# Optimization experiments

Hardware: AMD Instinct MI355X
Metric: run time of the kernel (lower is better)

Reference implementation:

```python
import jax, jax.numpy as jnp
import numpy as np

N_NODES = 100000
N_EDGES = 1600000
DIM = 64


def setup_inputs() -> dict:
    key = jax.random.key(0)
    ks = jax.random.split(key, 10)
    return {
        "h_real": jax.random.normal(ks[0], (N_NODES, DIM), dtype=jnp.float32),
        "h_imag": jax.random.normal(ks[1], (N_NODES, DIM), dtype=jnp.float32),
        "d": jax.random.uniform(ks[2], (N_NODES,), dtype=jnp.float32),
        "w_real": jax.random.normal(ks[3], (N_EDGES,), dtype=jnp.float32),
        "w_imag": jax.random.normal(ks[4], (N_EDGES,), dtype=jnp.float32),
        "src": jax.random.randint(ks[5], (N_EDGES,), 0, N_NODES, dtype=jnp.int32),
        "dst": jax.random.randint(ks[6], (N_EDGES,), 0, N_NODES, dtype=jnp.int32),
        "W1": jax.random.normal(ks[7], (DIM, DIM), dtype=jnp.float32) * (1.414 / np.sqrt(DIM)),
        "b1": jnp.zeros((DIM,), dtype=jnp.float32),
        "W2": jax.random.normal(ks[8], (DIM, DIM), dtype=jnp.float32) * (1.414 / np.sqrt(DIM)),
        "b2": jnp.zeros((DIM,), dtype=jnp.float32),
    }


def reference(h_real, h_imag, d, w_real, w_imag, src, dst, W1, b1, W2, b2):
    n = h_real.shape[0]
    # per-edge complex coefficient e = d_dst * d_src * (w_real + i w_imag)
    dd = d[dst] * d[src]                      # [E]
    e_r = (dd * w_real)[:, None]              # [E,1]
    e_i = (dd * w_imag)[:, None]              # [E,1]
    hr = h_real[src]                          # [E,D]
    hi = h_imag[src]                          # [E,D]
    # complex multiply e * h, fused single pass over edges
    m_r = e_r * hr - e_i * hi                 # [E,D]
    m_i = e_i * hr + e_r * hi                 # [E,D]
    z_real = jax.ops.segment_sum(m_r, dst, num_segments=n)  # [N,D]
    z_imag = jax.ops.segment_sum(m_i, dst, num_segments=n)  # [N,D]
    # note: original overwrites z_real first, then z_imag uses the NEW z_real
    zr = (z_real @ W1.T + b1) - (z_imag @ W2.T + b2)
    zi = (zr @ W2.T + b2) + (z_imag @ W1.T + b1)
    return zr, zi
```

## Files before the change

### kernel.cpp

```cpp
#include <hip/hip_runtime.h>
#include <hip/hip_bf16.h>

#define N_NODES 100000
#define N_EDGES 1600000
#define DIM 64

#define TILE 4096
#define B1 ((N_EDGES + TILE - 1) / TILE)
#define K1 ((N_NODES + 255) / 256)
#define NCOUNTS (K1 * B1)
#define SCAN_BLOCK 1024
#define NSB ((NCOUNTS + SCAN_BLOCK - 1) / SCAN_BLOCK)
#define PACKB4 ((N_NODES * DIM / 4 + 255) / 256)
#define PLACE_CAP 4736
#define NPW 8
#define PULLB (N_NODES / 32)

typedef __attribute__((ext_vector_type(8))) short bf16x8;
typedef __attribute__((ext_vector_type(4))) float f32x4;

#if defined(__has_builtin)
#if __has_builtin(__builtin_amdgcn_fdot2_f32_bf16)
#define HAVE_DOT2 1
typedef __attribute__((ext_vector_type(2))) __bf16 bf16x2v;
#endif
#endif


__device__ __forceinline__ unsigned pack_bf16x2(float lo, float hi) {
  unsigned ulo = (unsigned)__hip_bfloat16_raw(__float2bfloat16(lo)).x;
  unsigned uhi = (unsigned)__hip_bfloat16_raw(__float2bfloat16(hi)).x;
  return ulo | (uhi << 16);
}
__device__ __forceinline__ float unpack_lo(unsigned u) {
  return __int_as_float((int)(u << 16));
}
__device__ __forceinline__ float unpack_hi(unsigned u) {
  return __int_as_float((int)(u & 0xFFFF0000u));
}
__device__ __forceinline__ unsigned short f2bf(float x) {
  return __hip_bfloat16_raw(__float2bfloat16(x)).x;
}

__global__ __launch_bounds__(256) void setup_fused_kernel(
    const float* __restrict__ h_real, const float* __restrict__ h_imag,
    unsigned* __restrict__ hpack, const float* __restrict__ W1,
    const float* __restrict__ b1, const float* __restrict__ W2,
    const float* __restrict__ b2, unsigned short* __restrict__ At,
    float* __restrict__ cvec, const int* __restrict__ dst,
    int* __restrict__ counts) {
  const int bid = blockIdx.x;
  const int tid = threadIdx.x;
  if (bid < PACKB4) {
    const int i = bid * 256 + tid;
    const float4 hr = ((const float4*)h_real)[i];
    const float4 hi = ((const float4*)h_imag)[i];
    uint4 o;
    o.x = pack_bf16x2(hr.x, hi.x);
    o.y = pack_bf16x2(hr.y, hi.y);
    o.z = pack_bf16x2(hr.z, hi.z);
    o.w = pack_bf16x2(hr.w, hi.w);
    ((uint4*)hpack)[i] = o;
    return;
  }
  if (bid < PACKB4 + 64) {
    const int idx = (bid - PACKB4) * 256 + tid;
    if (idx < 128 * 128) {
      const int n = idx >> 7, k = idx & 127;
      float v;
      if (n < 64) {
        v = (k < 64) ? W1[n * 64 + k] : -W2[n * 64 + (k - 64)];
      } else {
        const int nn = n - 64;
        if (k < 64) {
          float s = 0.0f;
          for (int j = 0; j < 64; ++j) s += W1[j * 64 + k] * W2[nn * 64 + j];
          v = s;
        } else {
          const int kk = k - 64;
          float s = 0.0f;
          for (int j = 0; j < 64; ++j) s += W2[j * 64 + kk] * W2[nn * 64 + j];
          v = W1[nn * 64 + kk] - s;
        }
      }
      At[n * 128 + k] = f2bf(v);
    }
    if (idx < 128) {
      if (idx < 64) {
        cvec[idx] = b1[idx] - b2[idx];
      } else {
        const int nn = idx - 64;
        float s = 0.0f;
        for (int j = 0; j < 64; ++j) s += (b1[j] - b2[j]) * W2[nn * 64 + j];
        cvec[idx] = s + b1[nn] + b2[nn];
      }
    }
    return;
  }
  __shared__ int lh[K1];
  const int hb = bid - PACKB4 - 64;
  for (int i = tid; i < K1; i += 256) lh[i] = 0;
  __syncthreads();
  const int e0 = hb * TILE;
  const int e1 = min(e0 + TILE, N_EDGES);
  for (int e = e0 + tid; e < e1; e += 256) atomicAdd(&lh[dst[e] >> 8], 1);
  __syncthreads();
  for (int b = tid; b < K1; b += 256) counts[b * B1 + hb] = lh[b];
}

__global__ __launch_bounds__(SCAN_BLOCK) void scan1_kernel(
    int* __restrict__ cnt, int* __restrict__ bsum) {
  __shared__ int wsum[16];
  const int tid = threadIdx.x;
  const int lane = tid & 63;
  const int w = tid >> 6;
  const int i = blockIdx.x * SCAN_BLOCK + tid;
  const int orig = (i < NCOUNTS) ? cnt[i] : 0;
  int v = orig;
#pragma unroll
  for (int off = 1; off < 64; off <<= 1) {
    int t = __shfl_up(v, off);
    if (lane >= off) v += t;
  }
  if (lane == 63) wsum[w] = v;
  __syncthreads();
  if (w == 0) {
    int s = (lane < 16) ? wsum[lane] : 0;
#pragma unroll
    for (int off = 1; off < 16; off <<= 1) {
      int t = __shfl_up(s, off);
      if (lane >= off) s += t;
    }
    if (lane < 16) wsum[lane] = s;
  }
  __syncthreads();
  const int wex = (w == 0) ? 0 : wsum[w - 1];
  if (i < NCOUNTS) cnt[i] = wex + v - orig;
  if (tid == SCAN_BLOCK - 1) bsum[blockIdx.x] = wex + v;
}

__global__ __launch_bounds__(256) void scan2_kernel(
    const int* __restrict__ bsum, int* __restrict__ bpre) {
  __shared__ int wsum[4];
  const int tid = threadIdx.x;
  const int lane = tid & 63;
  const int w = tid >> 6;
  const int orig = (tid < NSB) ? bsum[tid] : 0;
  int v = orig;
#pragma unroll
  for (int off = 1; off < 64; off <<= 1) {
    int t = __shfl_up(v, off);
    if (lane >= off) v += t;
  }
  if (lane == 63) wsum[w] = v;
  __syncthreads();
  if (w == 0) {
    int s = (lane < 4) ? wsum[lane] : 0;
#pragma unroll
    for (int off = 1; off < 4; off <<= 1) {
      int t = __shfl_up(s, off);
      if (lane >= off) s += t;
    }
    if (lane < 4) wsum[lane] = s;
  }
  __syncthreads();
  const int wex = (w == 0) ? 0 : wsum[w - 1];
  if (tid < NSB) bpre[tid] = wex + v - orig;
}

__global__ __launch_bounds__(512) void partition_kernel(
    const int* __restrict__ src, const int* __restrict__ dst,
    const float* __restrict__ dvec,
    const float* __restrict__ w_real, const float* __restrict__ w_imag,
    const int* __restrict__ coffs, const int* __restrict__ bpre,
    unsigned long long* __restrict__ records) {
  __shared__ unsigned long long stage[TILE];
  __shared__ unsigned short sb[TILE];
  __shared__ int lhist[512];
  __shared__ int lbase[K1];
  __shared__ int lcur[K1];
  __shared__ int gbase[K1];
  __shared__ int wsum[8];
  const int tid = threadIdx.x;
  const int lane = tid & 63;
  const int w = tid >> 6;
  const int blk = blockIdx.x;
  const int e0 = blk * TILE;
  const int cnt_t = min(TILE, N_EDGES - e0);

  lhist[tid] = 0;
  __syncthreads();
  for (int j = tid; j < cnt_t; j += 512) atomicAdd(&lhist[dst[e0 + j] >> 8], 1);
  __syncthreads();
  const int myc = lhist[tid];
  int v = myc;
#pragma unroll
  for (int off = 1; off < 64; off <<= 1) {
    int t = __shfl_up(v, off);
    if (lane >= off) v += t;
  }
  if (lane == 63) wsum[w] = v;
  __syncthreads();
  if (w == 0) {
    int s = (lane < 8) ? wsum[lane] : 0;
#pragma unroll
    for (int off = 1; off < 8; off <<= 1) {
      int t = __shfl_up(s, off);
      if (lane >= off) s += t;
    }
    if (lane < 8) wsum[lane] = s;
  }
  __syncthreads();
  const int ex = v + ((w == 0) ? 0 : wsum[w - 1]) - myc;
  if (tid < K1) {
    lbase[tid] = ex;
    lcur[tid] = ex;
    const int ci = tid * B1 + blk;
    gbase[tid] = coffs[ci] + bpre[ci >> 10];
  }
  __syncthreads();

  for (int j = tid; j < cnt_t; j += 512) {
    const int e = e0 + j;
    const int t = dst[e];
    const int s = src[e];
    const int b = t >> 8;
    const float ds = dvec[s];
    const unsigned lo = (unsigned)s | ((unsigned)(t & 255) << 17);
    const unsigned hi = pack_bf16x2(ds * w_real[e], ds * w_imag[e]);
    const int r = atomicAdd(&lcur[b], 1);
    stage[r] = ((unsigned long long)hi << 32) | lo;
    sb[r] = (unsigned short)b;
  }
  __syncthreads();
  for (int i = tid; i < cnt_t; i += 512) {
    const int b = sb[i];
    records[gbase[b] + (i - lbase[b])] = stage[i];
  }
}

__global__ __launch_bounds__(256) void place_kernel(
    unsigned long long* __restrict__ records, const int* __restrict__ coffs,
    const int* __restrict__ bpre, int* __restrict__ inc) {
  const int b = blockIdx.x;
  const int tid = threadIdx.x;
  const int lane = tid & 63;
  const int w = tid >> 6;
  const int ci0 = b * B1;
  const int bstart = coffs[ci0] + bpre[ci0 >> 10];
  int bend;
  if (b == K1 - 1) {
    bend = N_EDGES;
  } else {
    const int ci1 = (b + 1) * B1;
    bend = coffs[ci1] + bpre[ci1 >> 10];
  }
  const int cnt = min(bend - bstart, PLACE_CAP);
  const int nbase = b << 8;
  const int nn = min(256, N_NODES - nbase);

  __shared__ unsigned long long stage[PLACE_CAP];
  __shared__ int ncnt[256];
  __shared__ int ncur[256];
  __shared__ int wsum[4];

  ncnt[tid] = 0;
  __syncthreads();
  for (int i = tid; i < cnt; i += 256) {
    const unsigned long long rec = records[bstart + i];
    stage[i] = rec;
    atomicAdd(&ncnt[((unsigned)rec >> 17) & 255], 1);
  }
  __syncthreads();
  const int myc = ncnt[tid];
  int v = myc;
#pragma unroll
  for (int off = 1; off < 64; off <<= 1) {
    int t = __shfl_up(v, off);
    if (lane >= off) v += t;
  }
  if (lane == 63) wsum[w] = v;
  __syncthreads();
  if (w == 0) {
    int s = (lane < 4) ? wsum[lane] : 0;
#pragma unroll
    for (int off = 1; off < 4; off <<= 1) {
      int t = __shfl_up(s, off);
      if (lane >= off) s += t;
    }
    if (lane < 4) wsum[lane] = s;
  }
  __syncthreads();
  const int incl = v + ((w == 0) ? 0 : wsum[w - 1]);
  const int base = bstart + incl - myc;
  ncur[tid] = base;
  if (tid < nn) inc[nbase + tid] = base + myc;
  __syncthreads();
  for (int i = tid; i < cnt; i += 256) {
    const unsigned long long rec = stage[i];
    const int pos = atomicAdd(&ncur[((unsigned)rec >> 17) & 255], 1);
    records[pos] = rec;
  }
}

__global__ __launch_bounds__(256, 8) void pull_fused_kernel(
    const uint2* __restrict__ records, const int* __restrict__ inc,
    const float* __restrict__ dvec, const unsigned* __restrict__ hpack,
    const unsigned short* __restrict__ At, const float* __restrict__ cvec,
    float* __restrict__ zr_out, float* __restrict__ zi_out) {
  __shared__ __align__(16) unsigned short zs[32][136];
  const int tid = threadIdx.x;
  const int lane = tid & 63;
  const int wave = tid >> 6;
  const int q4 = lane >> 4;
  const int m16 = lane & 15;
  const int node0 = blockIdx.x * 32;
  const unsigned* __restrict__ hb = hpack + 4 * m16;

#if HAVE_DOT2
#define DOT2(acc, w_, h_)                                                   \
  acc = __builtin_amdgcn_fdot2_f32_bf16(__builtin_bit_cast(bf16x2v, (w_)),  \
                                        __builtin_bit_cast(bf16x2v, (h_)),  \
                                        acc, false)
#else
#define DOT2(acc, w_, h_)                                                   \
  {                                                                         \
    const float _wl = unpack_lo(w_), _wh = unpack_hi(w_);                   \
    const float _hl = unpack_lo(h_), _hh = unpack_hi(h_);                   \
    acc += _wl * _hl + _wh * _hh;                                           \
  }
#endif

#define ACC4(RR)                                                            \
  {                                                                         \
    const unsigned wneg = (RR).y ^ 0x80000000u;                             \
    const unsigned wswp = ((RR).y >> 16) | ((RR).y << 16);                  \
    const uint4 hv = *reinterpret_cast<const uint4*>(                       \
        hb + (size_t)((RR).x & 0x1FFFF) * DIM);                             \
    DOT2(sr0, wneg, hv.x); DOT2(si0, wswp, hv.x);                           \
    DOT2(sr1, wneg, hv.y); DOT2(si1, wswp, hv.y);                           \
    DOT2(sr2, wneg, hv.z); DOT2(si2, wswp, hv.z);                           \
    DOT2(sr3, wneg, hv.w); DOT2(si3, wswp, hv.w);                           \
  }

  for (int j = 0; j < NPW; ++j) {
    const int n = node0 + wave * NPW + j;
    const int start = (n == 0) ? 0 : inc[n - 1];
    const int end = inc[n];
    const int deg = end - start;

    float sr0 = 0.f, sr1 = 0.f, sr2 = 0.f, sr3 = 0.f;
    float si0 = 0.f, si1 = 0.f, si2 = 0.f, si3 = 0.f;

    int p = start + q4;
    const int nfull = deg >> 2;
    int i = 0;
    for (; i + 2 <= nfull; i += 2) {
      const uint2 r0 = records[p];
      const uint2 r1 = records[p + 4];
      ACC4(r0);
      ACC4(r1);
      p += 8;
    }
    if (i < nfull) {
      const uint2 r0 = records[p];
      ACC4(r0);
      p += 4;
    }
    if (p < end) {
      const uint2 r0 = records[p];
      ACC4(r0);
    }

#define QRED(v)                  \
    v += __shfl_xor(v, 16);      \
    v += __shfl_xor(v, 32);
    QRED(sr0) QRED(sr1) QRED(sr2) QRED(sr3)
    QRED(si0) QRED(si1) QRED(si2) QRED(si3)
#undef QRED

    const float dn = dvec[n];
    if (lane < 16) {
      const int zl = wave * NPW + j;
      uint2 rv, iv;
      rv.x = pack_bf16x2(dn * sr0, dn * sr1);
      rv.y = pack_bf16x2(dn * sr2, dn * sr3);
      iv.x = pack_bf16x2(dn * si0, dn * si1);
      iv.y = pack_bf16x2(dn * si2, dn * si3);
      *reinterpret_cast<uint2*>(&zs[zl][4 * lane]) = rv;
      *reinterpret_cast<uint2*>(&zs[zl][64 + 4 * lane]) = iv;
    }
  }
#undef ACC4
#undef DOT2
  __syncthreads();

  {
    const int m = lane & 15;
    const int q = lane >> 4;
#pragma unroll
    for (int kk = 0; kk < 4; ++kk) {
      const int tt = wave + kk * 4;
      const int nh = tt >> 3;
      const int ft = tt & 7;

      bf16x8 a[4];
#pragma unroll
      for (int c = 0; c < 4; ++c)
        a[c] = *reinterpret_cast<const bf16x8*>(&zs[nh * 16 + m][c * 32 + q * 8]);

      f32x4 acc = (f32x4){0.f, 0.f, 0.f, 0.f};
      const unsigned short* brow = At + (size_t)(ft * 16 + m) * 128 + q * 8;
#pragma unroll
      for (int c = 0; c < 4; ++c) {
        bf16x8 bfrag = *reinterpret_cast<const bf16x8*>(brow + c * 32);
        acc = __builtin_amdgcn_mfma_f32_16x16x32_bf16(a[c], bfrag, acc, 0, 0, 0);
      }

      const int nf = ft * 16 + m;
      const float bias = cvec[nf];
      float* outp = (nf < 64) ? zr_out : zi_out;
      const int nnn = nf & 63;
#pragma unroll
      for (int r = 0; r < 4; ++r) {
        const int node = node0 + nh * 16 + q * 4 + r;
        outp[(size_t)node * 64 + nnn] = acc[r] + bias;
      }
    }
  }
}

extern "C" void kernel_launch(void* const* d_in, const int* in_sizes, int n_in,
                              void* d_out, int out_size, void* d_ws, size_t ws_size,
                              hipStream_t stream) {
  const float* h_real = (const float*)d_in[0];
  const float* h_imag = (const float*)d_in[1];
  const float* dvec   = (const float*)d_in[2];
  const float* w_real = (const float*)d_in[3];
  const float* w_imag = (const float*)d_in[4];
  const int*   src    = (const int*)d_in[5];
  const int*   dst    = (const int*)d_in[6];
  const float* W1     = (const float*)d_in[7];
  const float* b1     = (const float*)d_in[8];
  const float* W2     = (const float*)d_in[9];
  const float* b2     = (const float*)d_in[10];

  char* ws = (char*)d_ws;
  unsigned short* At = (unsigned short*)ws;
  float* cvec = (float*)(ws + 128 * 128 * 2);
  unsigned long long* records = (unsigned long long*)(ws + 33792);
  unsigned* hpack = (unsigned*)(ws + 33792 + (size_t)N_EDGES * 8);
  int* counts = (int*)(ws + 33792 + (size_t)N_EDGES * 8 + (size_t)N_NODES * DIM * 4);
  int* bsum = counts + NCOUNTS;
  int* bpre = bsum + NSB;
  int* inc  = bpre + NSB;

  float* zr_out = (float*)d_out;
  float* zi_out = zr_out + (size_t)N_NODES * DIM;

  setup_fused_kernel<<<PACKB4 + 64 + B1, 256, 0, stream>>>(
      h_real, h_imag, (unsigned*)hpack, W1, b1, W2, b2, At, cvec, dst, counts);
  scan1_kernel<<<NSB, SCAN_BLOCK, 0, stream>>>(counts, bsum);
  scan2_kernel<<<1, 256, 0, stream>>>(bsum, bpre);
  partition_kernel<<<B1, 512, 0, stream>>>(src, dst, dvec, w_real, w_imag,
                                           counts, bpre, records);
  place_kernel<<<K1, 256, 0, stream>>>(records, counts, bpre, inc);
  pull_fused_kernel<<<PULLB, 256, 0, stream>>>(
      (const uint2*)records, inc, dvec, hpack, At, cvec, zr_out, zi_out);
}
```

Measured before the change: 271.7 us.

## Restructure pull kernel: 16 nodes per 512-thread block, deeper gather unroll, staged stores

Result: faster. 265.1 us (-2.4%).

```diff
diff --git a/kernel.cpp b/kernel.cpp
--- a/kernel.cpp
+++ b/kernel.cpp
@@ -13,8 +13,7 @@
 #define NSB ((NCOUNTS + SCAN_BLOCK - 1) / SCAN_BLOCK)
 #define PACKB4 ((N_NODES * DIM / 4 + 255) / 256)
 #define PLACE_CAP 4736
-#define NPW 8
-#define PULLB (N_NODES / 32)
+#define PULLB (N_NODES / 16)
 
 typedef __attribute__((ext_vector_type(8))) short bf16x8;
 typedef __attribute__((ext_vector_type(4))) float f32x4;
@@ -303,18 +302,19 @@
   }
 }
 
-__global__ __launch_bounds__(256, 8) void pull_fused_kernel(
+__global__ __launch_bounds__(512, 8) void pull_fused_kernel(
     const uint2* __restrict__ records, const int* __restrict__ inc,
     const float* __restrict__ dvec, const unsigned* __restrict__ hpack,
     const unsigned short* __restrict__ At, const float* __restrict__ cvec,
     float* __restrict__ zr_out, float* __restrict__ zi_out) {
-  __shared__ __align__(16) unsigned short zs[32][136];
+  __shared__ __align__(16) unsigned short zs[16][136];
+  __shared__ __align__(16) float outbuf[16][132];
   const int tid = threadIdx.x;
   const int lane = tid & 63;
   const int wave = tid >> 6;
   const int q4 = lane >> 4;
   const int m16 = lane & 15;
-  const int node0 = blockIdx.x * 32;
+  const int node0 = blockIdx.x * 16;
   const unsigned* __restrict__ hb = hpack + 4 * m16;
 
 #if HAVE_DOT2
@@ -331,20 +331,21 @@
   }
 #endif
 
-#define ACC4(RR)                                                            \
+#define GATH(RR) \
+  (*reinterpret_cast<const uint4*>(hb + (size_t)((RR).x & 0x1FFFF) * DIM))
+
+#define DOTS(RR, HV)                                                        \
   {                                                                         \
     const unsigned wneg = (RR).y ^ 0x80000000u;                             \
     const unsigned wswp = ((RR).y >> 16) | ((RR).y << 16);                  \
-    const uint4 hv = *reinterpret_cast<const uint4*>(                       \
-        hb + (size_t)((RR).x & 0x1FFFF) * DIM);                             \
-    DOT2(sr0, wneg, hv.x); DOT2(si0, wswp, hv.x);                           \
-    DOT2(sr1, wneg, hv.y); DOT2(si1, wswp, hv.y);                           \
-    DOT2(sr2, wneg, hv.z); DOT2(si2, wswp, hv.z);                           \
-    DOT2(sr3, wneg, hv.w); DOT2(si3, wswp, hv.w);                           \
-  }
-
-  for (int j = 0; j < NPW; ++j) {
-    const int n = node0 + wave * NPW + j;
+    DOT2(sr0, wneg, (HV).x); DOT2(si0, wswp, (HV).x);                       \
+    DOT2(sr1, wneg, (HV).y); DOT2(si1, wswp, (HV).y);                       \
+    DOT2(sr2, wneg, (HV).z); DOT2(si2, wswp, (HV).z);                       \
+    DOT2(sr3, wneg, (HV).w); DOT2(si3, wswp, (HV).w);                       \
+  }
+
+  for (int j = 0; j < 2; ++j) {
+    const int n = node0 + wave * 2 + j;
     const int start = (n == 0) ? 0 : inc[n - 1];
     const int end = inc[n];
     const int deg = end - start;
@@ -355,21 +356,36 @@
     int p = start + q4;
     const int nfull = deg >> 2;
     int i = 0;
+    for (; i + 4 <= nfull; i += 4) {
+      const uint2 ra = records[p];
+      const uint2 rb = records[p + 4];
+      const uint2 rc = records[p + 8];
+      const uint2 rd = records[p + 12];
+      const uint4 ha = GATH(ra);
+      const uint4 hbv = GATH(rb);
+      const uint4 hc = GATH(rc);
+      const uint4 hd = GATH(rd);
+      DOTS(ra, ha) DOTS(rb, hbv) DOTS(rc, hc) DOTS(rd, hd)
+      p += 16;
+    }
     for (; i + 2 <= nfull; i += 2) {
-      const uint2 r0 = records[p];
-      const uint2 r1 = records[p + 4];
-      ACC4(r0);
-      ACC4(r1);
+      const uint2 ra = records[p];
+      const uint2 rb = records[p + 4];
+      const uint4 ha = GATH(ra);
+      const uint4 hbv = GATH(rb);
+      DOTS(ra, ha) DOTS(rb, hbv)
       p += 8;
     }
     if (i < nfull) {
-      const uint2 r0 = records[p];
-      ACC4(r0);
+      const uint2 ra = records[p];
+      const uint4 ha = GATH(ra);
+      DOTS(ra, ha)
       p += 4;
     }
     if (p < end) {
-      const uint2 r0 = records[p];
-      ACC4(r0);
+      const uint2 ra = records[p];
+      const uint4 ha = GATH(ra);
+      DOTS(ra, ha)
     }
 
 #define QRED(v)                  \
@@ -381,7 +397,7 @@
 
     const float dn = dvec[n];
     if (lane < 16) {
-      const int zl = wave * NPW + j;
+      const int zl = wave * 2 + j;
       uint2 rv, iv;
       rv.x = pack_bf16x2(dn * sr0, dn * sr1);
       rv.y = pack_bf16x2(dn * sr2, dn * sr3);
@@ -391,42 +407,44 @@
       *reinterpret_cast<uint2*>(&zs[zl][64 + 4 * lane]) = iv;
     }
   }
-#undef ACC4
+#undef DOTS
+#undef GATH
 #undef DOT2
   __syncthreads();
 
   {
+    const int t = wave;
     const int m = lane & 15;
     const int q = lane >> 4;
-#pragma unroll
-    for (int kk = 0; kk < 4; ++kk) {
-      const int tt = wave + kk * 4;
-      const int nh = tt >> 3;
-      const int ft = tt & 7;
-
-      bf16x8 a[4];
-#pragma unroll
-      for (int c = 0; c < 4; ++c)
-        a[c] = *reinterpret_cast<const bf16x8*>(&zs[nh * 16 + m][c * 32 + q * 8]);
-
-      f32x4 acc = (f32x4){0.f, 0.f, 0.f, 0.f};
-      const unsigned short* brow = At + (size_t)(ft * 16 + m) * 128 + q * 8;
-#pragma unroll
-      for (int c = 0; c < 4; ++c) {
-        bf16x8 bfrag = *reinterpret_cast<const bf16x8*>(brow + c * 32);
-        acc = __builtin_amdgcn_mfma_f32_16x16x32_bf16(a[c], bfrag, acc, 0, 0, 0);
-      }
-
-      const int nf = ft * 16 + m;
-      const float bias = cvec[nf];
-      float* outp = (nf < 64) ? zr_out : zi_out;
-      const int nnn = nf & 63;
-#pragma unroll
-      for (int r = 0; r < 4; ++r) {
-        const int node = node0 + nh * 16 + q * 4 + r;
-        outp[(size_t)node * 64 + nnn] = acc[r] + bias;
-      }
-    }
+
+    bf16x8 a[4];
+#pragma unroll
+    for (int c = 0; c < 4; ++c)
+      a[c] = *reinterpret_cast<const bf16x8*>(&zs[m][c * 32 + q * 8]);
+
+    f32x4 acc = (f32x4){0.f, 0.f, 0.f, 0.f};
+    const unsigned short* brow = At + (size_t)(t * 16 + m) * 128 + q * 8;
+#pragma unroll
+    for (int c = 0; c < 4; ++c) {
+      bf16x8 bfrag = *reinterpret_cast<const bf16x8*>(brow + c * 32);
+      acc = __builtin_amdgcn_mfma_f32_16x16x32_bf16(a[c], bfrag, acc, 0, 0, 0);
+    }
+
+    const int nf = t * 16 + m;
+    const float bias = cvec[nf];
+#pragma unroll
+    for (int r = 0; r < 4; ++r) outbuf[q * 4 + r][nf] = acc[r] + bias;
+  }
+  __syncthreads();
+
+  {
+    const int nl = tid >> 5;
+    const int c = tid & 31;
+    const float4 v = *reinterpret_cast<const float4*>(
+        &outbuf[nl][(c & 15) * 4 + (c >> 4) * 64]);
+    float* outp = (c < 16) ? zr_out : zi_out;
+    *reinterpret_cast<float4*>(
+        &outp[(size_t)(node0 + nl) * 64 + (c & 15) * 4]) = v;
   }
 }
 
@@ -465,6 +483,6 @@
   partition_kernel<<<B1, 512, 0, stream>>>(src, dst, dvec, w_real, w_imag,
                                            counts, bpre, records);
   place_kernel<<<K1, 256, 0, stream>>>(records, counts, bpre, inc);
-  pull_fused_kernel<<<PULLB, 256, 0, stream>>>(
+  pull_fused_kernel<<<PULLB, 512, 0, stream>>>(
       (const uint2*)records, inc, dvec, hpack, At, cvec, zr_out, zi_out);
 }
```
